# Kernel tuning notes

Measured on AMD Instinct MI355X. Metric: run time of the kernel, lower is better.

The kernel has to match this reference:

```python
import jax, jax.numpy as jnp
import numpy as np

N_WAY = 5
K_SHOT = 5
TEMPERATURE = 1.0
NEG = -1e9  # emulates 'column does not exist' for pad columns beyond umask_length
EPS = 1e-12  # matches torch F.normalize eps


def _l2n(x, axis):
    n = jnp.sqrt(jnp.sum(x * x, axis=axis, keepdims=True))
    return x / jnp.maximum(n, EPS)


def setup_inputs() -> dict:
    key = jax.random.key(0)
    k1, k2, k3, k4, k5 = jax.random.split(key, 5)
    b, c, h, w = 4, 64, 5, 5
    q, u = 75, 100
    support_xf = jax.random.normal(k1, (b, N_WAY * K_SHOT, c, h, w), jnp.float32)
    query_xf = jax.random.normal(k2, (b, q, c, h, w), jnp.float32)
    unlabeled_xf = jax.random.normal(k3, (b, u, c, h, w), jnp.float32)
    support_y = jax.random.randint(k4, (b, N_WAY * K_SHOT), 0, N_WAY)
    query_y = jax.random.randint(k5, (b, q), 0, N_WAY)
    return {"support_xf": support_xf, "support_y": support_y, "query_xf": query_xf,
            "query_y": query_y, "unlabeled_xf": unlabeled_xf}


def _forward(support_xf, query_xf, unlabeled_xf, query_y):
    b, q, c, h, w = query_xf.shape
    M_s = K_SHOT * h * w
    unl = unlabeled_xf.reshape(b, -1, c, h, w)
    u = unl.shape[1]
    M_u = u * h * w
    # pooled unlabeled local descriptors, flattened in (u, h, w) order -> [b, c, M_u]
    unl_feat = unl.transpose(0, 2, 1, 3, 4).reshape(b, c, M_u)
    # support -> [b, n_way, c, k_shot*h*w]
    sup = support_xf.reshape(b, N_WAY, K_SHOT, c, h, w).transpose(0, 1, 3, 2, 4, 5).reshape(b, N_WAY, c, M_s)
    # cosine similarity unlabeled -> support: [b, n_way, M_u, M_s]
    u2s = jnp.einsum('bwcn,bcm->bwmn', _l2n(sup, 2), _l2n(unl_feat, 1))
    pool = u2s.transpose(0, 2, 1, 3).reshape(b, M_u, N_WAY * M_s)
    s_nearest = jnp.argmax(pool, axis=1)          # per support loc: nearest unlabeled loc
    u_nearest = jnp.argmax(pool, axis=2)          # per unlabeled loc: nearest support loc
    mutual = jnp.take_along_axis(s_nearest, u_nearest, axis=1) == jnp.arange(M_u)[None, :]  # [b, M_u]
    # class with max similarity per unlabeled location
    cls = jnp.argmax(jnp.max(u2s, axis=-1), axis=1)  # [b, M_u]
    umask = jax.nn.one_hot(cls, N_WAY, dtype=jnp.float32).transpose(0, 2, 1) \
            * mutual[:, None, :].astype(jnp.float32)  # [b, n_way, M_u]
    counts = umask.sum(-1)                          # [b, n_way]
    L = counts.max()                                # umask_length (traced)
    # stream compaction via stable argsort of the 0/1 mask (preserves original order)
    order = jnp.argsort(-umask, axis=-1)            # jnp.argsort is stable
    pts = unl_feat.transpose(0, 2, 1)               # [b, M_u, c]
    gath = jnp.take_along_axis(pts[:, None, :, :], order[..., None], axis=2)  # [b, n_way, M_u, c]
    valid = (jnp.arange(M_u)[None, None, :] < counts[:, :, None]).astype(jnp.float32)
    comp = gath * valid[..., None]                  # rows beyond count are zeros (as in torch)
    s_cat = jnp.concatenate([sup, comp.transpose(0, 1, 3, 2)], axis=-1)  # [b, n_way, c, M_s+M_u]
    M_tot = M_s + M_u
    qn = _l2n(query_xf.reshape(b, q, c, h * w), 2)
    scn = _l2n(s_cat, 2)
    sim = jnp.einsum('bqcm,bwcn->bqwmn', qn, scn)   # [b, q, n_way, M_q, M_tot]
    sim = (sim + 1.0) * 0.5                          # FourLayer_64F branch
    # columns beyond umask_length don't exist in the torch dense tensor -> exclude from maxes
    pad = jnp.arange(M_tot)[None, None, None, None, :] >= (M_s + L)
    sim = jnp.where(pad, NEG, sim)
    M_q = h * w
    qm = sim.transpose(0, 1, 3, 2, 4).reshape(b, q, M_q, N_WAY * M_tot)
    support_nearest = jnp.argmax(qm, axis=2)        # [b, q, n_way*M_tot]
    query_nearest = jnp.argmax(qm, axis=3)          # [b, q, M_q]
    g = jnp.take_along_axis(support_nearest, query_nearest, axis=2)
    q_mask = (g == jnp.arange(M_q)[None, None, :]).astype(sim.dtype)  # mutual NN mask
    query_value = (jnp.max(sim, axis=-1) * q_mask[:, :, None, :]).sum(-1)  # [b, q, n_way]
    logits = query_value.reshape(b * q, N_WAY) / TEMPERATURE
    y = query_y.reshape(b * q)
    logp = jax.nn.log_softmax(logits, axis=-1)
    loss = -jnp.take_along_axis(logp, y[:, None], axis=1).mean()
    return loss


def reference(support_xf, support_y, query_xf, query_y, unlabeled_xf):
    return _forward(support_xf, query_xf, unlabeled_xf, query_y)
```

## Files before the change

### kernel.cpp

```cpp
#include <hip/hip_runtime.h>

#define NEGINF (-1e30f)

constexpr size_t OF_UNL  = 0;
constexpr size_t OF_SUP  = OF_UNL  + (size_t)4*2500*64;
constexpr size_t OF_SUPT = OF_SUP  + (size_t)4*5*125*64;
constexpr size_t OF_QT   = OF_SUPT + (size_t)4*5*64*128;
constexpr size_t OF_ROWV = OF_QT   + (size_t)300*64*25;
constexpr size_t OF_ROWI = OF_ROWV + (size_t)4*5*8*2500;
constexpr size_t OF_CVI  = OF_ROWI + (size_t)4*5*8*2500;
constexpr size_t OF_CMP  = OF_CVI  + (size_t)4*5*125*20*2;
constexpr size_t OF_CNT  = OF_CMP  + (size_t)4*5*2500;
constexpr size_t OF_UNEAR= OF_CNT  + 20;
constexpr size_t OF_SNEAR= OF_UNEAR+ 10000;
constexpr size_t OF_BV   = OF_SNEAR+ 2500;
constexpr size_t OF_BP   = OF_BV   + 37500;
constexpr size_t OF_AMX  = OF_BP   + 37500;

__global__ __launch_bounds__(256) void knorm(
    const float* __restrict__ sup, const float* __restrict__ qry,
    const float* __restrict__ unl,
    float* __restrict__ unl_n, float* __restrict__ sup_n,
    float* __restrict__ supT, float* __restrict__ qt)
{
    int gid = blockIdx.x * 256 + threadIdx.x;
    int loc = gid >> 4;
    int sub = gid & 15;
    if (loc >= 20000) return;

    const float* src;
    float* dst1; int dstr1;
    float* dst2 = nullptr;

    if (loc < 10000) {
        int b = loc / 2500, m = loc % 2500;
        int u = m / 25, hw = m % 25;
        src  = unl + ((size_t)(b*100 + u) * 64) * 25 + hw;
        dst1 = unl_n + (size_t)loc * 64; dstr1 = 1;
    } else if (loc < 12500) {
        int idx = loc - 10000;
        int b = idx / 625, r = idx % 625;
        int w = r / 125,  n = r % 125;
        int shot = n / 25, hw = n % 25;
        src  = sup + ((size_t)(b*25 + w*5 + shot) * 64) * 25 + hw;
        dst1 = sup_n + (size_t)idx * 64; dstr1 = 1;
        dst2 = supT + ((size_t)(b*5 + w) * 64) * 128 + n;
    } else {
        int idx = loc - 12500;
        int bq = idx / 25, mq = idx % 25;
        src  = qry + ((size_t)bq * 64) * 25 + mq;
        dst1 = qt + ((size_t)bq * 64) * 25 + mq; dstr1 = 25;
    }

    float v[4]; float ss = 0.f;
    int c0 = sub * 4;
#pragma unroll
    for (int j = 0; j < 4; ++j) { v[j] = src[(size_t)(c0 + j) * 25]; ss += v[j] * v[j]; }
#pragma unroll
    for (int msk = 1; msk < 16; msk <<= 1) ss += __shfl_xor(ss, msk);
    float sc = 1.f / fmaxf(sqrtf(ss), 1e-12f);
#pragma unroll
    for (int j = 0; j < 4; ++j) {
        float o = v[j] * sc;
        dst1[(size_t)(c0 + j) * dstr1] = o;
        if (dst2) dst2[(size_t)(c0 + j) * 128] = o;
    }
}

__global__ __launch_bounds__(256) void kb(
    const float* __restrict__ unl_n, const float* __restrict__ supT,
    float* __restrict__ rowv, int* __restrict__ rowi, float* __restrict__ colvi)
{
    int bid = blockIdx.x;
    int nc = bid & 3;
    int mb = (bid >> 2) % 20;
    int bw = bid / 80;
    int b  = bw / 5;
    int tid = threadIdx.x;
    int lane = tid & 63, wv = tid >> 6;

    __shared__ float uls[128 * 65];
    __shared__ float sls[64 * 36];
    __shared__ float sv_[4][32];
    __shared__ int   si_[4][32];

    int m0 = mb * 128;
    int n0 = nc * 32;

    for (int i = tid; i < 128 * 16; i += 256) {
        int row = i >> 4, c4 = (i & 15) * 4;
        int m = m0 + row;
        float4 x = make_float4(0.f, 0.f, 0.f, 0.f);
        if (m < 2500) x = *(const float4*)(unl_n + ((size_t)(b * 2500 + m)) * 64 + c4);
        uls[row * 65 + c4 + 0] = x.x;
        uls[row * 65 + c4 + 1] = x.y;
        uls[row * 65 + c4 + 2] = x.z;
        uls[row * 65 + c4 + 3] = x.w;
    }
    {
        int c = tid >> 2, q = tid & 3;
        const float* sp = supT + ((size_t)bw * 64 + c) * 128 + n0 + q * 8;
        float4 a = *(const float4*)sp;
        float4 d4 = *(const float4*)(sp + 4);
        float* d = &sls[c * 36 + q * 8];
        d[0] = a.x; d[1] = a.y; d[2] = a.z; d[3] = a.w;
        d[4] = d4.x; d[5] = d4.y; d[6] = d4.z; d[7] = d4.w;
    }
    __syncthreads();

    int ml = tid & 127;
    int m  = m0 + ml;
    int nh = tid >> 7;
    int nbase = nh * 16;
    int nn_total = (125 - n0) < 32 ? (125 - n0) : 32;
    const float* myrow = &uls[ml * 65];

    float acc[16];
#pragma unroll
    for (int j = 0; j < 16; ++j) acc[j] = 0.f;

    for (int c = 0; c < 64; ++c) {
        float uv = myrow[c];
        const float4* sr = (const float4*)&sls[c * 36 + nbase];
        float4 s0 = sr[0], s1 = sr[1], s2 = sr[2], s3 = sr[3];
        acc[0]  = fmaf(uv, s0.x, acc[0]);  acc[1]  = fmaf(uv, s0.y, acc[1]);
        acc[2]  = fmaf(uv, s0.z, acc[2]);  acc[3]  = fmaf(uv, s0.w, acc[3]);
        acc[4]  = fmaf(uv, s1.x, acc[4]);  acc[5]  = fmaf(uv, s1.y, acc[5]);
        acc[6]  = fmaf(uv, s1.z, acc[6]);  acc[7]  = fmaf(uv, s1.w, acc[7]);
        acc[8]  = fmaf(uv, s2.x, acc[8]);  acc[9]  = fmaf(uv, s2.y, acc[9]);
        acc[10] = fmaf(uv, s2.z, acc[10]); acc[11] = fmaf(uv, s2.w, acc[11]);
        acc[12] = fmaf(uv, s3.x, acc[12]); acc[13] = fmaf(uv, s3.y, acc[13]);
        acc[14] = fmaf(uv, s3.z, acc[14]); acc[15] = fmaf(uv, s3.w, acc[15]);
    }

    int nnloc = nn_total - nbase;
    nnloc = nnloc < 0 ? 0 : (nnloc > 16 ? 16 : nnloc);
    float rbv = NEGINF; int rbi = 0;
    for (int j = 0; j < nnloc; ++j)
        if (acc[j] > rbv) { rbv = acc[j]; rbi = n0 + nbase + j; }
    if (m < 2500) {
        int ck = nc * 2 + nh;
        rowv[((size_t)bw * 8 + ck) * 2500 + m] = rbv;
        rowi[((size_t)bw * 8 + ck) * 2500 + m] = rbi;
    }

#pragma unroll
    for (int j = 0; j < 16; ++j) {
        float v = (m < 2500 && (nbase + j) < nn_total) ? acc[j] : NEGINF;
        float vm = v;
#pragma unroll
        for (int s2 = 1; s2 < 64; s2 <<= 1) vm = fmaxf(vm, __shfl_xor(vm, s2));
        unsigned long long msk = __ballot(v == vm);
        int first = __ffsll((unsigned long long)msk) - 1;
        if (lane == 0) { sv_[wv][nbase + j] = vm; si_[wv][nbase + j] = m0 + (wv & 1) * 64 + first; }
    }
    __syncthreads();
    if (tid < nn_total) {
        int w0 = (tid < 16) ? 0 : 2;
        float v = sv_[w0][tid];     int vi = si_[w0][tid];
        float v2 = sv_[w0 + 1][tid]; int i2 = si_[w0 + 1][tid];
        if (v2 > v || (v2 == v && i2 < vi)) { v = v2; vi = i2; }
        float* cv = colvi + ((((size_t)bw) * 125 + (n0 + tid)) * 20 + mb) * 2;
        cv[0] = v; ((int*)cv)[1] = vi;
    }
}

__global__ __launch_bounds__(256) void kmerge(
    const float* __restrict__ rowv, const int* __restrict__ rowi,
    const float* __restrict__ colvi,
    int* __restrict__ unear, int* __restrict__ snear)
{
    int it = blockIdx.x * 256 + threadIdx.x;
    if (it < 10000) {
        int b = it / 2500, m = it % 2500;
        float bv = NEGINF; int bi = 0;
#pragma unroll
        for (int w = 0; w < 5; ++w) {
#pragma unroll
            for (int ck = 0; ck < 8; ++ck) {
                size_t o = (((size_t)(b * 5 + w)) * 8 + ck) * 2500 + m;
                float v = rowv[o];
                if (v > bv) { bv = v; bi = w * 125 + rowi[o]; }
            }
        }
        unear[it] = bi;
    } else if (it < 12500) {
        int idx = it - 10000;
        const float* p = colvi + (size_t)idx * 40;
        float bv = NEGINF; int bi = 0x7fffffff;
        for (int mb2 = 0; mb2 < 20; ++mb2) {
            float v = p[mb2 * 2]; int vi = ((const int*)p)[mb2 * 2 + 1];
            if (v > bv || (v == bv && vi < bi)) { bv = v; bi = vi; }
        }
        snear[idx] = bi;
    }
}

__global__ __launch_bounds__(256) void kcmp(
    const int* __restrict__ unear, const int* __restrict__ snear,
    int* __restrict__ cmp, int* __restrict__ cntg)
{
    int p = blockIdx.x;
    int b = p / 5, way = p % 5;
    int tid = threadIdx.x, lane = tid & 63, wv = tid >> 6;
    __shared__ unsigned long long masks[40];
    __shared__ int base[40];

    for (int ch = wv; ch < 40; ch += 4) {
        int m = ch * 64 + lane;
        bool ok = false;
        if (m < 2500) {
            int un = unear[b * 2500 + m];
            ok = (un / 125 == way) && (snear[b * 625 + un] == m);
        }
        unsigned long long msk = __ballot(ok ? 1 : 0);
        if (lane == 0) masks[ch] = msk;
    }
    __syncthreads();
    if (tid == 0) {
        int s = 0;
        for (int ch = 0; ch < 40; ++ch) { base[ch] = s; s += __popcll(masks[ch]); }
        cntg[p] = s;
    }
    __syncthreads();
    for (int ch = wv; ch < 40; ch += 4) {
        unsigned long long msk = masks[ch];
        if ((msk >> lane) & 1ull) {
            int pre = __popcll(msk & ((1ull << lane) - 1ull));
            cmp[(size_t)p * 2500 + base[ch] + pre] = ch * 64 + lane;
        }
    }
}

__global__ __launch_bounds__(256) void kc1(
    const float* __restrict__ qt, const float* __restrict__ sup_n,
    const float* __restrict__ unl_n, const int* __restrict__ cmp,
    const int* __restrict__ cntg,
    float* __restrict__ bvg, int* __restrict__ bpg,
    unsigned char* __restrict__ amaxg)
{
    int bid = blockIdx.x;
    int w = bid % 5, bq = bid / 5;
    int b = bq / 75;
    int tid = threadIdx.x;

    const float* qtb = qt + (size_t)bq * 64 * 25;

    int L = 0;
#pragma unroll
    for (int i = 0; i < 20; ++i) { int v = cntg[i]; L = L > v ? L : v; }
    int cntw = 0, wb = 0;
#pragma unroll
    for (int w2 = 0; w2 < 5; ++w2) {
        int c2 = cntg[b * 5 + w2];
        if (w2 < w) wb += 125 + c2;
        if (w2 == w) cntw = c2;
    }
    int cw = 125 + cntw;

    __shared__ float simb[25 * 257];
    __shared__ float redv[8][25];
    __shared__ int   redp[8][25];

    int rg = tid / 25, rq = tid % 25;
    float bv1 = NEGINF; int bp1 = 0x7fffffff;

    for (int c0 = 0; c0 < cw; c0 += 256) {
        int n = c0 + tid;
        if (n < cw) {
            const float* colp;
            if (n < 125) colp = sup_n + (((size_t)(b * 5 + w)) * 125 + n) * 64;
            else {
                int m = cmp[((size_t)(b * 5 + w)) * 2500 + (n - 125)];
                colp = unl_n + ((size_t)(b * 2500 + m)) * 64;
            }
            float acc[25];
#pragma unroll
            for (int i = 0; i < 25; ++i) acc[i] = 0.f;
            for (int c = 0; c < 64; c += 4) {
                float4 cv = *(const float4*)(colp + c);
                const float* qr = qtb + c * 25;
#pragma unroll
                for (int mq = 0; mq < 25; ++mq) {
                    acc[mq] = fmaf(cv.x, qr[mq],      acc[mq]);
                    acc[mq] = fmaf(cv.y, qr[25 + mq], acc[mq]);
                    acc[mq] = fmaf(cv.z, qr[50 + mq], acc[mq]);
                    acc[mq] = fmaf(cv.w, qr[75 + mq], acc[mq]);
                }
            }
            float cmax = NEGINF; int cam = 0;
#pragma unroll
            for (int mq = 0; mq < 25; ++mq) {
                float s = (acc[mq] + 1.0f) * 0.5f;
                if (s > cmax) { cmax = s; cam = mq; }
                simb[mq * 257 + tid] = s;
            }
            amaxg[(size_t)bq * 3200 + (wb + n)] = (unsigned char)cam;
        }
        __syncthreads();
        if (tid < 200) {
            int base = rg * 32;
            for (int i = 0; i < 32; ++i) {
                int n2 = c0 + base + i;
                if (n2 < cw) {
                    float s = simb[rq * 257 + base + i];
                    if (s > bv1) { bv1 = s; bp1 = ((w * 2625 + n2) << 12) | (wb + n2); }
                }
            }
        }
        __syncthreads();
    }

    if (tid < 200) { redv[rg][rq] = bv1; redp[rg][rq] = bp1; }
    __syncthreads();
    if (tid < 25) {
        float v = redv[0][tid]; int p = redp[0][tid];
#pragma unroll
        for (int g = 1; g < 8; ++g)
            if (redv[g][tid] > v) { v = redv[g][tid]; p = redp[g][tid]; }
        if (L > cntw) {
            int pp = ((w * 2625 + 125 + cntw) << 12) | 0xFFF;
            if (0.5f > v || (0.5f == v && pp < p)) { v = 0.5f; p = pp; }
        }
        size_t o = ((size_t)bq * 5 + w) * 25 + tid;
        bvg[o] = v; bpg[o] = p;
    }
}

__global__ __launch_bounds__(64) void kce(
    const float* __restrict__ bvg, const int* __restrict__ bpg,
    const unsigned char* __restrict__ amaxg, const int* __restrict__ qy,
    float* __restrict__ out)
{
    int bq = blockIdx.x;
    int tid = threadIdx.x;
    __shared__ float qmask[25];
    __shared__ float lg[5];
    if (tid < 25) {
        float v = NEGINF; int p = 0x7fffffff;
#pragma unroll
        for (int w = 0; w < 5; ++w) {
            size_t o = ((size_t)bq * 5 + w) * 25 + tid;
            float v2 = bvg[o]; int p2 = bpg[o];
            if (v2 > v || (v2 == v && p2 < p)) { v = v2; p = p2; }
        }
        int pos = p & 0xFFF;
        int g = (pos == 0xFFF) ? 0 : (int)amaxg[(size_t)bq * 3200 + pos];
        qmask[tid] = (g == tid) ? 1.0f : 0.0f;
    }
    __syncthreads();
    if (tid < 5) {
        float s = 0.f;
#pragma unroll
        for (int mq = 0; mq < 25; ++mq)
            s += bvg[((size_t)bq * 5 + tid) * 25 + mq] * qmask[mq];
        lg[tid] = s;
    }
    __syncthreads();
    if (tid == 0) {
        int y = qy[bq];
        float mx = lg[0];
#pragma unroll
        for (int w = 1; w < 5; ++w) mx = fmaxf(mx, lg[w]);
        float se = 0.f;
#pragma unroll
        for (int w = 0; w < 5; ++w) se += expf(lg[w] - mx);
        float loss = -(lg[y] - mx - logf(se));
        atomicAdd(out, loss * (1.0f / 300.0f));
    }
}

extern "C" void kernel_launch(void* const* d_in, const int* in_sizes, int n_in,
                              void* d_out, int out_size, void* d_ws, size_t ws_size,
                              hipStream_t stream)
{
    const float* sup = (const float*)d_in[0];
    const float* qry = (const float*)d_in[2];
    const int*   qy  = (const int*)d_in[3];
    const float* unl = (const float*)d_in[4];

    float* ws    = (float*)d_ws;
    float* unl_n = ws + OF_UNL;
    float* sup_n = ws + OF_SUP;
    float* supT  = ws + OF_SUPT;
    float* qt    = ws + OF_QT;
    float* rowv  = ws + OF_ROWV;
    int*   rowi  = (int*)(ws + OF_ROWI);
    float* colvi = ws + OF_CVI;
    int*   cmp   = (int*)(ws + OF_CMP);
    int*   cntg  = (int*)(ws + OF_CNT);
    int*   unear = (int*)(ws + OF_UNEAR);
    int*   snear = (int*)(ws + OF_SNEAR);
    float* bvg   = ws + OF_BV;
    int*   bpg   = (int*)(ws + OF_BP);
    unsigned char* amaxg = (unsigned char*)(ws + OF_AMX);

    hipMemsetAsync(d_out, 0, sizeof(float), stream);

    hipLaunchKernelGGL(knorm, dim3(1250), dim3(256), 0, stream,
                       sup, qry, unl, unl_n, sup_n, supT, qt);
    hipLaunchKernelGGL(kb, dim3(1600), dim3(256), 0, stream,
                       unl_n, supT, rowv, rowi, colvi);
    hipLaunchKernelGGL(kmerge, dim3(49), dim3(256), 0, stream,
                       rowv, rowi, colvi, unear, snear);
    hipLaunchKernelGGL(kcmp, dim3(20), dim3(256), 0, stream,
                       unear, snear, cmp, cntg);
    hipLaunchKernelGGL(kc1, dim3(1500), dim3(256), 0, stream,
                       qt, sup_n, unl_n, cmp, cntg, bvg, bpg, amaxg);
    hipLaunchKernelGGL(kce, dim3(300), dim3(64), 0, stream,
                       bvg, bpg, amaxg, qy, (float*)d_out);
}
```

Measured before the change: 181.4 us.

## Stage normalized query tile in LDS with row-major layout for float4 reads

The normalized query tile is now stored row-major ([25][64]) instead of channel-major, and kc1 copies each block's query tile into shared memory once. The inner dot-product loop then reads float4 broadcasts from LDS instead of scalar global loads through cache. This removes repeated uniform global loads in the hot loop, at the cost of 6.4KB more LDS per block and one extra barrier.

```diff
diff --git a/kernel.cpp b/kernel.cpp
--- a/kernel.cpp
+++ b/kernel.cpp
@@ -29,27 +29,27 @@
     if (loc >= 20000) return;
 
     const float* src;
-    float* dst1; int dstr1;
+    float* dst1;
     float* dst2 = nullptr;
 
     if (loc < 10000) {
         int b = loc / 2500, m = loc % 2500;
         int u = m / 25, hw = m % 25;
         src  = unl + ((size_t)(b*100 + u) * 64) * 25 + hw;
-        dst1 = unl_n + (size_t)loc * 64; dstr1 = 1;
+        dst1 = unl_n + (size_t)loc * 64;
     } else if (loc < 12500) {
         int idx = loc - 10000;
         int b = idx / 625, r = idx % 625;
         int w = r / 125,  n = r % 125;
         int shot = n / 25, hw = n % 25;
         src  = sup + ((size_t)(b*25 + w*5 + shot) * 64) * 25 + hw;
-        dst1 = sup_n + (size_t)idx * 64; dstr1 = 1;
+        dst1 = sup_n + (size_t)idx * 64;
         dst2 = supT + ((size_t)(b*5 + w) * 64) * 128 + n;
     } else {
         int idx = loc - 12500;
         int bq = idx / 25, mq = idx % 25;
         src  = qry + ((size_t)bq * 64) * 25 + mq;
-        dst1 = qt + ((size_t)bq * 64) * 25 + mq; dstr1 = 25;
+        dst1 = qt + ((size_t)bq * 25 + mq) * 64;
     }
 
     float v[4]; float ss = 0.f;
@@ -62,7 +62,7 @@
 #pragma unroll
     for (int j = 0; j < 4; ++j) {
         float o = v[j] * sc;
-        dst1[(size_t)(c0 + j) * dstr1] = o;
+        dst1[c0 + j] = o;
         if (dst2) dst2[(size_t)(c0 + j) * 128] = o;
     }
 }
@@ -244,7 +244,7 @@
     int b = bq / 75;
     int tid = threadIdx.x;
 
-    const float* qtb = qt + (size_t)bq * 64 * 25;
+    const float* qtb = qt + (size_t)bq * 1600;
 
     int L = 0;
 #pragma unroll
@@ -258,12 +258,16 @@
     }
     int cw = 125 + cntw;
 
+    __shared__ float qls[25 * 64];
     __shared__ float simb[25 * 257];
     __shared__ float redv[8][25];
     __shared__ int   redp[8][25];
 
+    for (int i = tid; i < 1600; i += 256) qls[i] = qtb[i];
+
     int rg = tid / 25, rq = tid % 25;
     float bv1 = NEGINF; int bp1 = 0x7fffffff;
+    __syncthreads();
 
     for (int c0 = 0; c0 < cw; c0 += 256) {
         int n = c0 + tid;
@@ -277,15 +281,16 @@
             float acc[25];
 #pragma unroll
             for (int i = 0; i < 25; ++i) acc[i] = 0.f;
-            for (int c = 0; c < 64; c += 4) {
-                float4 cv = *(const float4*)(colp + c);
-                const float* qr = qtb + c * 25;
+#pragma unroll
+            for (int cg = 0; cg < 16; ++cg) {
+                float4 cv = *(const float4*)(colp + cg * 4);
 #pragma unroll
                 for (int mq = 0; mq < 25; ++mq) {
-                    acc[mq] = fmaf(cv.x, qr[mq],      acc[mq]);
-                    acc[mq] = fmaf(cv.y, qr[25 + mq], acc[mq]);
-                    acc[mq] = fmaf(cv.z, qr[50 + mq], acc[mq]);
-                    acc[mq] = fmaf(cv.w, qr[75 + mq], acc[mq]);
+                    float4 qv = *(const float4*)&qls[mq * 64 + cg * 4];
+                    acc[mq] = fmaf(cv.x, qv.x, acc[mq]);
+                    acc[mq] = fmaf(cv.y, qv.y, acc[mq]);
+                    acc[mq] = fmaf(cv.z, qv.z, acc[mq]);
+                    acc[mq] = fmaf(cv.w, qv.w, acc[mq]);
                 }
             }
             float cmax = NEGINF; int cam = 0;
```

After: 184.7 us. About the same (+1.8%).
